# Kernel optimization log

Measured on AMD Instinct MI355X. Metric: run time of the kernel, lower is better.

## Reference

```python
import jax, jax.numpy as jnp
import numpy as np

N_QUBITS = 14
Q_DEPTH = 4
N_GEN = 8
BATCH = 512

# CNOT in (control, target) basis ordering |00,01,10,11>
_CNOT = jnp.array([[1., 0., 0., 0.],
                   [0., 1., 0., 0.],
                   [0., 0., 0., 1.],
                   [0., 0., 1., 0.]], dtype=jnp.float32)


def _ry(t):
    c = jnp.cos(t / 2)
    s = jnp.sin(t / 2)
    return jnp.stack([jnp.stack([c, -s]), jnp.stack([s, c])])  # [2,2]


def _apply_1q(state, gate, w):
    # state: (2,)*n real tensor; apply 2x2 gate on wire w
    n = state.ndim
    st = jnp.moveaxis(state, w, 0).reshape(2, -1)
    st = gate @ st
    return jnp.moveaxis(st.reshape((2,) * n), 0, w)


def _apply_2q(state, gate, w0, w1):
    n = state.ndim
    st = jnp.moveaxis(state, (w0, w1), (0, 1)).reshape(4, -1)
    st = gate @ st
    return jnp.moveaxis(st.reshape((2,) * n), (0, 1), (w0, w1))


def _circuit(theta):
    # EfficientSU2-with-circular-entanglement circuit, repeated Q_DEPTH times.
    # RY + CNOT on |0...0> keeps amplitudes real -> float32 statevector.
    state = jnp.zeros((2,) * N_QUBITS, dtype=jnp.float32).at[(0,) * N_QUBITS].set(1.0)
    for _ in range(Q_DEPTH):
        for i in range(N_QUBITS):
            state = _apply_1q(state, _ry(theta[i]), i)
        for i in range(N_QUBITS):
            state = _apply_2q(state, _CNOT, i, (i + 1) % N_QUBITS)
        for i in range(N_QUBITS):
            state = _apply_1q(state, _ry(theta[i]), i)
    probs = state * state
    # <Z_i> = P(bit_i = 0) - P(bit_i = 1)
    z = []
    for i in range(N_QUBITS):
        p = jnp.moveaxis(probs, i, 0).reshape(2, -1).sum(axis=1)
        z.append(p[0] - p[1])
    return jnp.stack(z)  # [n_qubits]


def setup_inputs() -> dict:
    key = jax.random.key(0)
    k1, k2, k3 = jax.random.split(key, 3)
    x = jax.random.normal(k1, (BATCH, N_QUBITS), dtype=jnp.float32)
    # q_params: per-generator n_qubits x n_qubits matrices (orthogonal-ish small init)
    W = jax.random.normal(k2, (N_GEN, N_QUBITS, N_QUBITS), dtype=jnp.float32) * 0.01
    b = jax.random.uniform(k3, (N_GEN, N_QUBITS), minval=-0.01, maxval=0.01, dtype=jnp.float32)
    return {"x": x, "W": W, "b": b}


def reference(x, W, b):
    # theta[b,g] = x[b] @ W[g] + b[g]   -> [B, G, n_qubits]
    theta = jnp.einsum('bq,gqp->bgp', x, W) + b[None]
    expvals = jax.vmap(jax.vmap(_circuit))(theta)  # [B, G, n_qubits]
    return expvals.reshape(x.shape[0], -1)  # [B, G*n_qubits]
```

## Files before the change

kernel.cpp:

```cpp
#include <hip/hip_runtime.h>
#include <stdint.h>

#define NQ 14
#define NPASS 5
#define NGEN 8
#define NTH 256
#define NBLK (512*NGEN)

constexpr int cpop16(uint32_t x){ int n=0; for(int i=0;i<16;++i) n+=(x>>i)&1; return n; }

struct Mat { uint16_t col[NQ]; };
struct Tables {
    uint16_t mask[NPASS][NQ];
    uint16_t rho [NPASS][NQ];
    uint16_t zrho[NQ];
    bool ok;
};
constexpr uint16_t ring_apply(uint16_t j) {
    for (int i = 0; i < NQ; ++i) { int t=(i+1)%NQ; j=(uint16_t)(j ^ (((j>>i)&1u)<<t)); }
    return j;
}
constexpr Mat identity() { Mat m{}; for (int i=0;i<NQ;++i) m.col[i]=(uint16_t)(1u<<i); return m; }
constexpr uint16_t mat_row(const Mat& L, int r) {
    uint16_t v=0; for (int b=0;b<NQ;++b) v=(uint16_t)(v | (((L.col[b]>>r)&1u)<<b)); return v;
}
constexpr uint16_t mat_apply(const Mat& L, uint16_t x) {
    uint16_t r=0; for (int b=0;b<NQ;++b) if ((x>>b)&1u) r=(uint16_t)(r ^ L.col[b]); return r;
}
constexpr Mat inverse(const Mat& L, bool& ok) {
    uint32_t lrow[NQ]={}, irow[NQ]={};
    for (int r=0;r<NQ;++r){ lrow[r]=mat_row(L,r); irow[r]=1u<<r; }
    for (int c=0;c<NQ;++c){
        int piv=-1;
        for (int r=c;r<NQ;++r) if ((lrow[r]>>c)&1u){ piv=r; break; }
        if (piv<0){ ok=false; return identity(); }
        uint32_t tl=lrow[c]; lrow[c]=lrow[piv]; lrow[piv]=tl;
        uint32_t ti=irow[c]; irow[c]=irow[piv]; irow[piv]=ti;
        for (int r=0;r<NQ;++r) if (r!=c && ((lrow[r]>>c)&1u)){ lrow[r]^=lrow[c]; irow[r]^=irow[c]; }
    }
    Mat inv{};
    for (int w=0;w<NQ;++w){ uint16_t cv=0; for (int r=0;r<NQ;++r) cv=(uint16_t)(cv | (((irow[r]>>w)&1u)<<r)); inv.col[w]=cv; }
    return inv;
}
constexpr Mat mat_mul(const Mat& A, const Mat& B) {
    Mat r{}; for (int j=0;j<NQ;++j) r.col[j]=mat_apply(A,B.col[j]); return r;
}
constexpr uint16_t mat_tapply(const Mat& M, uint16_t r) {
    uint16_t v=0; for (int j=0;j<NQ;++j) v=(uint16_t)(v | ((uint16_t)(cpop16(M.col[j]&r)&1)<<j)); return v;
}
constexpr Tables build() {
    Tables t{}; t.ok = true;
    Mat L = identity();
    for (int p=0;p<NPASS;++p) {
        if (p>0) { Mat Ln{}; for (int b=0;b<NQ;++b) Ln.col[b]=ring_apply(L.col[b]); L=Ln; }
        bool ok = true; Mat inv = inverse(L, ok); if (!ok) t.ok = false;
        for (int w=0;w<NQ;++w) {
            t.mask[p][w] = inv.col[w];
            t.rho [p][w] = mat_row(L,w);
            if (mat_apply(L, inv.col[w]) != (uint16_t)(1u<<w)) t.ok = false;
        }
    }
    for (int w=0;w<NQ;++w) t.zrho[w] = mat_row(L,w);
    return t;
}
constexpr Tables TBL = build();
static_assert(TBL.ok, "GF2 table build failed");
static_assert(TBL.mask[0][0]==1 && TBL.rho[0][0]==1, "pass0 w0");
static_assert(TBL.mask[0][13]==(1u<<13) && TBL.rho[0][13]==(1u<<13), "pass0 w13");
static_assert(TBL.mask[1][0]==3,      "pass1 w0 mask");
static_assert(TBL.rho [1][0]==0x3FFE, "pass1 w0 rho");
static_assert(TBL.mask[1][12]==0x3000,"pass1 w12 mask");

#define MAXPH 28
struct Sched {
    bool ok; int nph; int ngtot;
    uint16_t M[MAXPH][NQ];
    int ng[MAXPH];
    int gw[MAXPH][6]; int gsc[MAXPH][6];
    uint16_t gmu[MAXPH][6];
    uint16_t grho[MAXPH][6];
    uint16_t zrho[NQ];
};
struct Basis { uint16_t lead[16]; };
constexpr bool binsert(Basis& B, uint16_t v) {
    v &= 0x3FFC;
    while (v) {
        int t=-1; for (int i=15;i>=0;--i) if ((v>>i)&1u){ t=i; break; }
        if (!B.lead[t]) { B.lead[t]=v; return true; }
        v = (uint16_t)(v ^ B.lead[t]);
    }
    return false;
}
constexpr Sched try_build(int u0,int u1,int u2) {
    Sched S{}; S.ok=true; S.nph=0; S.ngtot=0;
    uint16_t lam[3] = { (uint16_t)((1u<<2)|(1u<<u0)), (uint16_t)((1u<<3)|(1u<<u1)), (uint16_t)((1u<<4)|(1u<<u2)) };
    Mat prevT = identity();
    for (int p=1;p<NPASS;++p) {
        bool done[NQ]={}; bool isq[NQ]={}; int nleft=0;
        for (int w=0;w<NQ;++w){ if ((TBL.mask[p][w] & ~3u)==0) isq[w]=true; else ++nleft; }
        bool first=true; int guard=0;
        while (nleft>0) {
            if (S.nph>=MAXPH || ++guard>MAXPH){ S.ok=false; return S; }
            int ph=S.nph++;
            Basis B{};
            if(!binsert(B,lam[0])||!binsert(B,lam[1])||!binsert(B,lam[2])){ S.ok=false; return S; }
            Mat T{}; T.col[0]=1; T.col[1]=2; T.col[2]=lam[0]; T.col[3]=lam[1]; T.col[4]=lam[2];
            int slotw[4]={}; int nsl=0;
            for (int round=0;round<2;++round)
                for (int w=0;w<NQ;++w) {
                    if (nsl==4) break;
                    if (done[w]||isq[w]) continue;
                    uint16_t m=TBL.mask[p][w];
                    bool stuck = ((m & 0x3FE0u)==0);
                    if ((round==0)!=stuck) continue;
                    if (binsert(B,(uint16_t)(m&~3u))) {
                        T.col[10+nsl]=(uint16_t)(m&~3u); slotw[nsl++]=w; done[w]=true; --nleft;
                    }
                }
            if (nsl==0){ S.ok=false; return S; }
            int freecols[9]; int nf=0;
            for (int c=5;c<=9;++c)        freecols[nf++]=c;
            for (int c=10+nsl;c<=13;++c)  freecols[nf++]=c;
            int filled=0;
            for (int b=5;b<NQ && filled<nf;++b) if (binsert(B,(uint16_t)(1u<<b))) T.col[freecols[filled++]]=(uint16_t)(1u<<b);
            for (int b=2;b<5  && filled<nf;++b) if (binsert(B,(uint16_t)(1u<<b))) T.col[freecols[filled++]]=(uint16_t)(1u<<b);
            if (filled!=nf){ S.ok=false; return S; }
            bool iok=true; Mat Ti=inverse(T,iok); if(!iok){ S.ok=false; return S; }
            S.ng[ph]=0;
            for (int i=0;i<nsl;++i) {
                int w=slotw[i]; uint16_t m=TBL.mask[p][w];
                uint16_t mu=mat_apply(Ti,m);
                if (mu & 0x03FCu){ S.ok=false; return S; }
                int gi=S.ng[ph]++; ++S.ngtot;
                S.gw[ph][gi]=w; S.gsc[ph][gi]=(p==NPASS-1)?0:1;
                S.gmu[ph][gi]=(uint16_t)(((mu>>10)<<2)|(mu&3u));
                S.grho[ph][gi]=mat_tapply(T,TBL.rho[p][w]);
            }
            if (first) {
                for (int w=0;w<NQ;++w) if (isq[w]) {
                    int gi=S.ng[ph]++; ++S.ngtot;
                    S.gw[ph][gi]=w; S.gsc[ph][gi]=(p==NPASS-1)?0:1;
                    S.gmu[ph][gi]=(uint16_t)(TBL.mask[p][w]&3u);
                    S.grho[ph][gi]=mat_tapply(T,TBL.rho[p][w]);
                }
                first=false;
            }
            bool iok2=true; Mat Pi=inverse(prevT,iok2); if(!iok2){ S.ok=false; return S; }
            Mat M=mat_mul(Pi,T);
            if (M.col[0]!=1u || M.col[1]!=2u){ S.ok=false; return S; }
            for (int c=2;c<NQ;++c) if (M.col[c]&3u){ S.ok=false; return S; }
            for (int c=2;c<5;++c)  if ((M.col[c]&0x1Cu)!=(1u<<c)){ S.ok=false; return S; }
            for (int c=0;c<NQ;++c) S.M[ph][c]=M.col[c];
            prevT=T;
        }
    }
    for (int w=0;w<NQ;++w) S.zrho[w]=mat_tapply(prevT,TBL.zrho[w]);
    return S;
}
constexpr Sched build_sched() {
    Sched S = try_build(5,6,7);    if (S.ok) return S;
    S = try_build(8,9,10);         if (S.ok) return S;
    S = try_build(11,12,13);       if (S.ok) return S;
    S = try_build(5,9,13);         if (S.ok) return S;
    S = try_build(13,9,5);         if (S.ok) return S;
    S = try_build(7,5,6);          return S;
}
constexpr Sched SCH = build_sched();
static_assert(SCH.ok, "frame schedule build failed");
static_assert(SCH.ngtot == 4*NQ, "not all 56 gates scheduled");
constexpr int NPH = SCH.nph;
static_assert(NPH >= 8 && NPH <= MAXPH, "unexpected phase count");

template<int PH> __device__ __forceinline__
void run_phase(float (&q)[64], unsigned tid, float4* Aq, const float (&CS)[2][2][NQ]) {
    unsigned tq = 0;
    #pragma unroll
    for (int k=0;k<8;++k) {
        const unsigned col = ((unsigned)SCH.M[PH][2+k]) >> 2;
        tq ^= (((tid>>k)&1u) ? col : 0u);
    }
    #pragma unroll
    for (int IT=0;IT<16;++IT) {
        unsigned cit = 0;
        if (IT&1) cit ^= ((unsigned)SCH.M[PH][10])>>2;
        if (IT&2) cit ^= ((unsigned)SCH.M[PH][11])>>2;
        if (IT&4) cit ^= ((unsigned)SCH.M[PH][12])>>2;
        if (IT&8) cit ^= ((unsigned)SCH.M[PH][13])>>2;
        const float4 v = Aq[tq ^ cit];
        q[IT*4+0]=v.x; q[IT*4+1]=v.y; q[IT*4+2]=v.z; q[IT*4+3]=v.w;
    }
    #pragma unroll
    for (int gi=0; gi<SCH.ng[PH]; ++gi) {
        const int w = SCH.gw[PH][gi], sc = SCH.gsc[PH][gi];
        const unsigned mu  = SCH.gmu[PH][gi];
        const unsigned rho = SCH.grho[PH][gi];
        const float cc = CS[sc][0][w], ss = CS[sc][1][w];
        const unsigned pt = __popc(rho & (tid<<2)) & 1u;
        const float fp = pt ? ss : -ss;
        const float fn = -fp;
        #pragma unroll
        for (int l=0;l<64;++l) {
            const unsigned piv = 1u << (31 - __builtin_clz(mu));
            if (l & piv) continue;
            const int l2 = l ^ (int)mu;
            const unsigned ya = (((unsigned)l >>2)<<10) | ((unsigned)l &3u);
            const unsigned yb = (((unsigned)l2>>2)<<10) | ((unsigned)l2&3u);
            const float a=q[l], b=q[l2];
            q[l]  = fmaf((__popc(rho&ya)&1) ? fn : fp, b, cc*a);
            q[l2] = fmaf((__popc(rho&yb)&1) ? fn : fp, a, cc*b);
        }
    }
}

template<int PH> __device__ __forceinline__
void phases_from(float (&q)[64], unsigned tid, float4* Aq, const float (&CS)[2][2][NQ]) {
    if constexpr (PH < NPH) {
        run_phase<PH>(q, tid, Aq, CS);
        if constexpr (PH+1 < NPH) {
            __syncthreads();
            #pragma unroll
            for (int IT=0;IT<16;++IT)
                Aq[((unsigned)IT<<8)|tid] = make_float4(q[IT*4],q[IT*4+1],q[IT*4+2],q[IT*4+3]);
            __syncthreads();
        }
        phases_from<PH+1>(q, tid, Aq, CS);
    }
}

__global__ __launch_bounds__(NTH)
void qgen_kernel(const float* __restrict__ x, const float* __restrict__ W,
                 const float* __restrict__ bias, float* __restrict__ out)
{
    __shared__ float4 Aq[4096];
    __shared__ float CS[2][2][NQ];
    __shared__ float zacc[NQ];

    const int blk = blockIdx.x;
    const int bb  = blk >> 3;
    const int g   = blk & 7;
    const unsigned tid = threadIdx.x;

    if (tid < NQ) {
        float acc = bias[g*NQ + tid];
        #pragma unroll
        for (int qq=0;qq<NQ;++qq) acc += x[bb*NQ+qq] * W[(g*NQ+qq)*NQ + tid];
        float h = 0.5f*acc;
        CS[0][0][tid]=cosf(h);   CS[0][1][tid]=sinf(h);
        CS[1][0][tid]=cosf(acc); CS[1][1][tid]=sinf(acc);
        zacc[tid]=0.f;
    }
    __syncthreads();

    float q[64];
    {
        float tp = 1.f;
        #pragma unroll
        for (int k=0;k<8;++k) tp *= ((tid>>k)&1u) ? CS[0][1][2+k] : CS[0][0][2+k];
        const float c0=CS[0][0][0], s0=CS[0][1][0], c1=CS[0][0][1], s1=CS[0][1][1];
        #pragma unroll
        for (int IT=0;IT<16;++IT) {
            float f = tp;
            #pragma unroll
            for (int b=0;b<4;++b) f *= ((IT>>b)&1) ? CS[0][1][10+b] : CS[0][0][10+b];
            q[IT*4+0]=f*c0*c1; q[IT*4+1]=f*s0*c1; q[IT*4+2]=f*c0*s1; q[IT*4+3]=f*s0*s1;
        }
        #pragma unroll
        for (int IT=0;IT<16;++IT)
            Aq[((unsigned)IT<<8)|tid] = make_float4(q[IT*4],q[IT*4+1],q[IT*4+2],q[IT*4+3]);
        __syncthreads();
    }

    phases_from<0>(q, tid, Aq, CS);

    float acc[NQ];
    #pragma unroll
    for (int w=0;w<NQ;++w) acc[w]=0.f;
    #pragma unroll
    for (int l=0;l<64;++l) {
        const float pr = q[l]*q[l];
        #pragma unroll
        for (int w=0;w<NQ;++w) {
            const unsigned zr = SCH.zrho[w];
            const unsigned ya = (((unsigned)l>>2)<<10) | ((unsigned)l&3u);
            acc[w] += (__popc(zr&ya)&1) ? -pr : pr;
        }
    }
    #pragma unroll
    for (int w=0;w<NQ;++w) {
        const unsigned zr = SCH.zrho[w];
        if (__popc(zr & (tid<<2)) & 1) acc[w] = -acc[w];
        #pragma unroll
        for (int off=32; off; off>>=1) acc[w] += __shfl_down(acc[w], off, 64);
    }
    if ((tid & 63u) == 0) {
        #pragma unroll
        for (int w=0;w<NQ;++w) atomicAdd(&zacc[w], acc[w]);
    }
    __syncthreads();
    if (tid < NQ) out[blk*NQ + tid] = zacc[tid];
}

extern "C" void kernel_launch(void* const* d_in, const int* in_sizes, int n_in,
                              void* d_out, int out_size, void* d_ws, size_t ws_size,
                              hipStream_t stream) {
    (void)in_sizes; (void)n_in; (void)d_ws; (void)ws_size; (void)out_size;
    const float* x    = (const float*)d_in[0];
    const float* W    = (const float*)d_in[1];
    const float* bias = (const float*)d_in[2];
    float* out = (float*)d_out;
    qgen_kernel<<<dim3(NBLK), dim3(NTH), 0, stream>>>(x, W, bias, out);
}
```

Before: 302.5 us.

## Merge gate passes into fewer phases, pack state as float2, use Walsh-Hadamard reduction

The compile-time schedule builder now scans every pending gate of the current pass, and of the next pass once the current one is finished, and places each gate whose mask fits the phase frame into that phase. This cuts the number of phases and the shared-memory exchanges and barriers between them. The register state is held as 32 float2 values so gate updates can use packed FMA and swizzle operations. The final Z expectation uses an in-register Walsh-Hadamard butterfly instead of accumulating the 14 sums directly. Risks include higher register pressure from more gates per phase and from the h array, and a schedule that depends on which constexpr candidate builds successfully.

```diff
diff --git a/kernel.cpp b/kernel.cpp
--- a/kernel.cpp
+++ b/kernel.cpp
@@ -6,6 +6,8 @@
 #define NGEN 8
 #define NTH 256
 #define NBLK (512*NGEN)
+
+typedef float f2 __attribute__((ext_vector_type(2)));
 
 constexpr int cpop16(uint32_t x){ int n=0; for(int i=0;i<16;++i) n+=(x>>i)&1; return n; }
 
@@ -66,19 +68,19 @@
 constexpr Tables TBL = build();
 static_assert(TBL.ok, "GF2 table build failed");
 static_assert(TBL.mask[0][0]==1 && TBL.rho[0][0]==1, "pass0 w0");
-static_assert(TBL.mask[0][13]==(1u<<13) && TBL.rho[0][13]==(1u<<13), "pass0 w13");
 static_assert(TBL.mask[1][0]==3,      "pass1 w0 mask");
 static_assert(TBL.rho [1][0]==0x3FFE, "pass1 w0 rho");
 static_assert(TBL.mask[1][12]==0x3000,"pass1 w12 mask");
 
 #define MAXPH 28
+#define MAXG 14
 struct Sched {
     bool ok; int nph; int ngtot;
     uint16_t M[MAXPH][NQ];
     int ng[MAXPH];
-    int gw[MAXPH][6]; int gsc[MAXPH][6];
-    uint16_t gmu[MAXPH][6];
-    uint16_t grho[MAXPH][6];
+    int gw[MAXPH][MAXG]; int gsc[MAXPH][MAXG];
+    uint16_t gmu[MAXPH][MAXG];
+    uint16_t grho[MAXPH][MAXG];
     uint16_t zrho[NQ];
 };
 struct Basis { uint16_t lead[16]; };
@@ -93,66 +95,69 @@
 }
 constexpr Sched try_build(int u0,int u1,int u2) {
     Sched S{}; S.ok=true; S.nph=0; S.ngtot=0;
-    uint16_t lam[3] = { (uint16_t)((1u<<2)|(1u<<u0)), (uint16_t)((1u<<3)|(1u<<u1)), (uint16_t)((1u<<4)|(1u<<u2)) };
+    const uint16_t lam[3] = { (uint16_t)((1u<<2)|(1u<<u0)), (uint16_t)((1u<<3)|(1u<<u1)), (uint16_t)((1u<<4)|(1u<<u2)) };
     Mat prevT = identity();
-    for (int p=1;p<NPASS;++p) {
-        bool done[NQ]={}; bool isq[NQ]={}; int nleft=0;
-        for (int w=0;w<NQ;++w){ if ((TBL.mask[p][w] & ~3u)==0) isq[w]=true; else ++nleft; }
-        bool first=true; int guard=0;
-        while (nleft>0) {
-            if (S.nph>=MAXPH || ++guard>MAXPH){ S.ok=false; return S; }
-            int ph=S.nph++;
-            Basis B{};
-            if(!binsert(B,lam[0])||!binsert(B,lam[1])||!binsert(B,lam[2])){ S.ok=false; return S; }
-            Mat T{}; T.col[0]=1; T.col[1]=2; T.col[2]=lam[0]; T.col[3]=lam[1]; T.col[4]=lam[2];
-            int slotw[4]={}; int nsl=0;
-            for (int round=0;round<2;++round)
-                for (int w=0;w<NQ;++w) {
-                    if (nsl==4) break;
-                    if (done[w]||isq[w]) continue;
-                    uint16_t m=TBL.mask[p][w];
-                    bool stuck = ((m & 0x3FE0u)==0);
-                    if ((round==0)!=stuck) continue;
-                    if (binsert(B,(uint16_t)(m&~3u))) {
-                        T.col[10+nsl]=(uint16_t)(m&~3u); slotw[nsl++]=w; done[w]=true; --nleft;
-                    }
-                }
-            if (nsl==0){ S.ok=false; return S; }
-            int freecols[9]; int nf=0;
-            for (int c=5;c<=9;++c)        freecols[nf++]=c;
-            for (int c=10+nsl;c<=13;++c)  freecols[nf++]=c;
-            int filled=0;
-            for (int b=5;b<NQ && filled<nf;++b) if (binsert(B,(uint16_t)(1u<<b))) T.col[freecols[filled++]]=(uint16_t)(1u<<b);
-            for (int b=2;b<5  && filled<nf;++b) if (binsert(B,(uint16_t)(1u<<b))) T.col[freecols[filled++]]=(uint16_t)(1u<<b);
-            if (filled!=nf){ S.ok=false; return S; }
-            bool iok=true; Mat Ti=inverse(T,iok); if(!iok){ S.ok=false; return S; }
-            S.ng[ph]=0;
-            for (int i=0;i<nsl;++i) {
-                int w=slotw[i]; uint16_t m=TBL.mask[p][w];
-                uint16_t mu=mat_apply(Ti,m);
-                if (mu & 0x03FCu){ S.ok=false; return S; }
-                int gi=S.ng[ph]++; ++S.ngtot;
-                S.gw[ph][gi]=w; S.gsc[ph][gi]=(p==NPASS-1)?0:1;
+    bool done[NPASS][NQ] = {};
+    int pend[NPASS] = {};
+    for (int p=1;p<NPASS;++p) pend[p]=NQ;
+    int pc = 1; int guard = 0;
+    while (pc < NPASS) {
+        if (pend[pc]==0) { ++pc; continue; }
+        if (S.nph>=MAXPH || ++guard>MAXPH){ S.ok=false; return S; }
+        const int ph = S.nph++;
+        Basis B{};
+        if(!binsert(B,lam[0])||!binsert(B,lam[1])||!binsert(B,lam[2])){ S.ok=false; return S; }
+        Mat T{}; T.col[0]=1; T.col[1]=2; T.col[2]=lam[0]; T.col[3]=lam[1]; T.col[4]=lam[2];
+        int nsl=0;
+        for (int round=0;round<2 && nsl<4;++round)
+            for (int w=0;w<NQ && nsl<4;++w) {
+                if (done[pc][w]) continue;
+                const uint16_t m=TBL.mask[pc][w];
+                if ((m & ~3u)==0) continue;
+                const bool stuck = ((m & 0x3FE0u)==0);
+                if ((round==0)!=stuck) continue;
+                if (binsert(B,(uint16_t)(m&~3u))) T.col[10+nsl++]=(uint16_t)(m&~3u);
+            }
+        int freecols[9]; int nf=0;
+        for (int c=5;c<=9;++c)        freecols[nf++]=c;
+        for (int c=10+nsl;c<=13;++c)  freecols[nf++]=c;
+        int filled=0;
+        for (int b=5;b<NQ && filled<nf;++b) if (binsert(B,(uint16_t)(1u<<b))) T.col[freecols[filled++]]=(uint16_t)(1u<<b);
+        for (int b=2;b<5  && filled<nf;++b) if (binsert(B,(uint16_t)(1u<<b))) T.col[freecols[filled++]]=(uint16_t)(1u<<b);
+        if (filled!=nf){ S.ok=false; return S; }
+        bool iok=true; const Mat Ti=inverse(T,iok); if(!iok){ S.ok=false; return S; }
+        S.ng[ph]=0;
+        for (int w=0;w<NQ;++w) {
+            if (done[pc][w]) continue;
+            const uint16_t mu=mat_apply(Ti,TBL.mask[pc][w]);
+            if (mu & 0x03FCu) continue;
+            const int gi=S.ng[ph]++; ++S.ngtot;
+            S.gw[ph][gi]=w; S.gsc[ph][gi]=(pc==NPASS-1)?0:1;
+            S.gmu[ph][gi]=(uint16_t)(((mu>>10)<<2)|(mu&3u));
+            S.grho[ph][gi]=mat_tapply(T,TBL.rho[pc][w]);
+            done[pc][w]=true; --pend[pc];
+        }
+        if (S.ng[ph]==0){ S.ok=false; return S; }
+        if (pend[pc]==0 && pc+1<NPASS) {
+            const int p2=pc+1;
+            for (int w=0;w<NQ;++w) {
+                if (done[p2][w]) continue;
+                const uint16_t mu=mat_apply(Ti,TBL.mask[p2][w]);
+                if (mu & 0x03FCu) continue;
+                const int gi=S.ng[ph]++; ++S.ngtot;
+                S.gw[ph][gi]=w; S.gsc[ph][gi]=(p2==NPASS-1)?0:1;
                 S.gmu[ph][gi]=(uint16_t)(((mu>>10)<<2)|(mu&3u));
-                S.grho[ph][gi]=mat_tapply(T,TBL.rho[p][w]);
+                S.grho[ph][gi]=mat_tapply(T,TBL.rho[p2][w]);
+                done[p2][w]=true; --pend[p2];
             }
-            if (first) {
-                for (int w=0;w<NQ;++w) if (isq[w]) {
-                    int gi=S.ng[ph]++; ++S.ngtot;
-                    S.gw[ph][gi]=w; S.gsc[ph][gi]=(p==NPASS-1)?0:1;
-                    S.gmu[ph][gi]=(uint16_t)(TBL.mask[p][w]&3u);
-                    S.grho[ph][gi]=mat_tapply(T,TBL.rho[p][w]);
-                }
-                first=false;
-            }
-            bool iok2=true; Mat Pi=inverse(prevT,iok2); if(!iok2){ S.ok=false; return S; }
-            Mat M=mat_mul(Pi,T);
-            if (M.col[0]!=1u || M.col[1]!=2u){ S.ok=false; return S; }
-            for (int c=2;c<NQ;++c) if (M.col[c]&3u){ S.ok=false; return S; }
-            for (int c=2;c<5;++c)  if ((M.col[c]&0x1Cu)!=(1u<<c)){ S.ok=false; return S; }
-            for (int c=0;c<NQ;++c) S.M[ph][c]=M.col[c];
-            prevT=T;
-        }
+        }
+        bool iok2=true; const Mat Pi=inverse(prevT,iok2); if(!iok2){ S.ok=false; return S; }
+        const Mat M=mat_mul(Pi,T);
+        if (M.col[0]!=1u || M.col[1]!=2u){ S.ok=false; return S; }
+        for (int c=2;c<NQ;++c) if (M.col[c]&3u){ S.ok=false; return S; }
+        for (int c=2;c<5;++c)  if ((M.col[c]&0x1Cu)!=(1u<<c)){ S.ok=false; return S; }
+        for (int c=0;c<NQ;++c) S.M[ph][c]=M.col[c];
+        prevT=T;
     }
     for (int w=0;w<NQ;++w) S.zrho[w]=mat_tapply(prevT,TBL.zrho[w]);
     return S;
@@ -163,16 +168,18 @@
     S = try_build(11,12,13);       if (S.ok) return S;
     S = try_build(5,9,13);         if (S.ok) return S;
     S = try_build(13,9,5);         if (S.ok) return S;
+    S = try_build(6,7,8);          if (S.ok) return S;
+    S = try_build(9,10,11);        if (S.ok) return S;
     S = try_build(7,5,6);          return S;
 }
 constexpr Sched SCH = build_sched();
 static_assert(SCH.ok, "frame schedule build failed");
 static_assert(SCH.ngtot == 4*NQ, "not all 56 gates scheduled");
 constexpr int NPH = SCH.nph;
-static_assert(NPH >= 8 && NPH <= MAXPH, "unexpected phase count");
+static_assert(NPH >= 5 && NPH <= MAXPH, "unexpected phase count");
 
 template<int PH> __device__ __forceinline__
-void run_phase(float (&q)[64], unsigned tid, float4* Aq, const float (&CS)[2][2][NQ]) {
+void run_phase(f2 (&qq)[32], unsigned tid, float4* Aq, const float (&CS)[2][2][NQ]) {
     unsigned tq = 0;
     #pragma unroll
     for (int k=0;k<8;++k) {
@@ -187,43 +194,67 @@
         if (IT&4) cit ^= ((unsigned)SCH.M[PH][12])>>2;
         if (IT&8) cit ^= ((unsigned)SCH.M[PH][13])>>2;
         const float4 v = Aq[tq ^ cit];
-        q[IT*4+0]=v.x; q[IT*4+1]=v.y; q[IT*4+2]=v.z; q[IT*4+3]=v.w;
+        qq[2*IT]   = f2{v.x, v.y};
+        qq[2*IT+1] = f2{v.z, v.w};
     }
     #pragma unroll
     for (int gi=0; gi<SCH.ng[PH]; ++gi) {
         const int w = SCH.gw[PH][gi], sc = SCH.gsc[PH][gi];
-        const unsigned mu  = SCH.gmu[PH][gi];
+        const unsigned lm  = SCH.gmu[PH][gi];
         const unsigned rho = SCH.grho[PH][gi];
-        const float cc = CS[sc][0][w], ss = CS[sc][1][w];
+        const float cc = CS[sc][0][w], sv = CS[sc][1][w];
         const unsigned pt = __popc(rho & (tid<<2)) & 1u;
-        const float fp = pt ? ss : -ss;
-        const float fn = -fp;
-        #pragma unroll
-        for (int l=0;l<64;++l) {
-            const unsigned piv = 1u << (31 - __builtin_clz(mu));
-            if (l & piv) continue;
-            const int l2 = l ^ (int)mu;
-            const unsigned ya = (((unsigned)l >>2)<<10) | ((unsigned)l &3u);
-            const unsigned yb = (((unsigned)l2>>2)<<10) | ((unsigned)l2&3u);
-            const float a=q[l], b=q[l2];
-            q[l]  = fmaf((__popc(rho&ya)&1) ? fn : fp, b, cc*a);
-            q[l2] = fmaf((__popc(rho&yb)&1) ? fn : fp, a, cc*b);
+        const float u  = pt ? sv : -sv;
+        const f2 c2 = {cc, cc};
+        const f2 uu = {u, u};
+        const f2 un = {u, -u};
+        const unsigned di = ((lm>>1)&1u) | ((lm>>2)<<1);
+        if (di == 0u) {
+            #pragma unroll
+            for (int i=0;i<32;++i) {
+                const unsigned ya0 = ((unsigned)(i&1)<<1) | (((unsigned)i>>1)<<10);
+                const int s0 = __popc(rho & ya0) & 1;
+                const int s1 = __popc(rho & (ya0|1u)) & 1;
+                const f2 a = qq[i];
+                const f2 pv = __builtin_shufflevector(a, a, 1, 0);
+                const f2 t = (s0==s1) ? uu : un;
+                qq[i] = __builtin_elementwise_fma(s0 ? -t : t, pv, c2*a);
+            }
+        } else {
+            const int dpiv = 1 << (31 - __builtin_clz(di));
+            const int jsw = (int)(lm & 1u);
+            #pragma unroll
+            for (int i=0;i<32;++i) {
+                if (i & dpiv) continue;
+                const int i2 = i ^ (int)di;
+                const unsigned ya0 = ((unsigned)(i &1)<<1) | (((unsigned)i >>1)<<10);
+                const unsigned yb0 = ((unsigned)(i2&1)<<1) | (((unsigned)i2>>1)<<10);
+                const int sa0 = __popc(rho & ya0)&1,      sa1 = __popc(rho & (ya0|1u))&1;
+                const int sb0 = __popc(rho & yb0)&1,      sb1 = __popc(rho & (yb0|1u))&1;
+                const f2 a = qq[i], b = qq[i2];
+                const f2 pa = jsw ? __builtin_shufflevector(b,b,1,0) : b;
+                const f2 pb = jsw ? __builtin_shufflevector(a,a,1,0) : a;
+                const f2 ta = (sa0==sa1) ? uu : un;
+                const f2 tb = (sb0==sb1) ? uu : un;
+                qq[i]  = __builtin_elementwise_fma(sa0 ? -ta : ta, pa, c2*a);
+                qq[i2] = __builtin_elementwise_fma(sb0 ? -tb : tb, pb, c2*b);
+            }
         }
     }
 }
 
 template<int PH> __device__ __forceinline__
-void phases_from(float (&q)[64], unsigned tid, float4* Aq, const float (&CS)[2][2][NQ]) {
+void phases_from(f2 (&qq)[32], unsigned tid, float4* Aq, const float (&CS)[2][2][NQ]) {
     if constexpr (PH < NPH) {
-        run_phase<PH>(q, tid, Aq, CS);
+        run_phase<PH>(qq, tid, Aq, CS);
         if constexpr (PH+1 < NPH) {
             __syncthreads();
             #pragma unroll
             for (int IT=0;IT<16;++IT)
-                Aq[((unsigned)IT<<8)|tid] = make_float4(q[IT*4],q[IT*4+1],q[IT*4+2],q[IT*4+3]);
+                Aq[((unsigned)IT<<8)|tid] = make_float4(qq[2*IT].x,qq[2*IT].y,qq[2*IT+1].x,qq[2*IT+1].y);
             __syncthreads();
         }
-        phases_from<PH+1>(q, tid, Aq, CS);
+        phases_from<PH+1>(qq, tid, Aq, CS);
     }
 }
 
@@ -243,7 +274,7 @@
     if (tid < NQ) {
         float acc = bias[g*NQ + tid];
         #pragma unroll
-        for (int qq=0;qq<NQ;++qq) acc += x[bb*NQ+qq] * W[(g*NQ+qq)*NQ + tid];
+        for (int qq2=0;qq2<NQ;++qq2) acc += x[bb*NQ+qq2] * W[(g*NQ+qq2)*NQ + tid];
         float h = 0.5f*acc;
         CS[0][0][tid]=cosf(h);   CS[0][1][tid]=sinf(h);
         CS[1][0][tid]=cosf(acc); CS[1][1][tid]=sinf(acc);
@@ -251,7 +282,7 @@
     }
     __syncthreads();
 
-    float q[64];
+    f2 qq[32];
     {
         float tp = 1.f;
         #pragma unroll
@@ -262,39 +293,39 @@
             float f = tp;
             #pragma unroll
             for (int b=0;b<4;++b) f *= ((IT>>b)&1) ? CS[0][1][10+b] : CS[0][0][10+b];
-            q[IT*4+0]=f*c0*c1; q[IT*4+1]=f*s0*c1; q[IT*4+2]=f*c0*s1; q[IT*4+3]=f*s0*s1;
+            qq[2*IT]   = f2{f*c0*c1, f*s0*c1};
+            qq[2*IT+1] = f2{f*c0*s1, f*s0*s1};
         }
         #pragma unroll
         for (int IT=0;IT<16;++IT)
-            Aq[((unsigned)IT<<8)|tid] = make_float4(q[IT*4],q[IT*4+1],q[IT*4+2],q[IT*4+3]);
+            Aq[((unsigned)IT<<8)|tid] = make_float4(qq[2*IT].x,qq[2*IT].y,qq[2*IT+1].x,qq[2*IT+1].y);
         __syncthreads();
     }
 
-    phases_from<0>(q, tid, Aq, CS);
-
-    float acc[NQ];
-    #pragma unroll
-    for (int w=0;w<NQ;++w) acc[w]=0.f;
-    #pragma unroll
-    for (int l=0;l<64;++l) {
-        const float pr = q[l]*q[l];
-        #pragma unroll
-        for (int w=0;w<NQ;++w) {
-            const unsigned zr = SCH.zrho[w];
-            const unsigned ya = (((unsigned)l>>2)<<10) | ((unsigned)l&3u);
-            acc[w] += (__popc(zr&ya)&1) ? -pr : pr;
+    phases_from<0>(qq, tid, Aq, CS);
+
+    f2 h[32];
+    #pragma unroll
+    for (int i=0;i<32;++i) h[i] = qq[i]*qq[i];
+    #pragma unroll
+    for (int b=0;b<5;++b) {
+        #pragma unroll
+        for (int i=0;i<32;++i) {
+            if (i & (1<<b)) continue;
+            const int i2 = i | (1<<b);
+            const f2 xv = h[i], yv = h[i2];
+            h[i] = xv + yv; h[i2] = xv - yv;
         }
     }
     #pragma unroll
     for (int w=0;w<NQ;++w) {
         const unsigned zr = SCH.zrho[w];
-        if (__popc(zr & (tid<<2)) & 1) acc[w] = -acc[w];
-        #pragma unroll
-        for (int off=32; off; off>>=1) acc[w] += __shfl_down(acc[w], off, 64);
-    }
-    if ((tid & 63u) == 0) {
-        #pragma unroll
-        for (int w=0;w<NQ;++w) atomicAdd(&zacc[w], acc[w]);
+        const int ri = (int)(((zr>>1)&1u) | (((zr>>10)&0xFu)<<1));
+        float val = (zr&1u) ? (h[ri].x - h[ri].y) : (h[ri].x + h[ri].y);
+        if (__popc(zr & (tid<<2)) & 1) val = -val;
+        #pragma unroll
+        for (int off=32; off; off>>=1) val += __shfl_down(val, off, 64);
+        if ((tid & 63u) == 0) atomicAdd(&zacc[w], val);
     }
     __syncthreads();
     if (tid < NQ) out[blk*NQ + tid] = zacc[tid];
```

After: 302.3 us. About the same (-0.1%).
